# Kernel optimization log

Hardware: AMD Instinct MI355X
Metric: run time of the kernel (lower is better)

## Reference

```python
import jax, jax.numpy as jnp
import numpy as np

N_NODES = 10000
N_EDGES = 320000
NUM_NEIGHBORS = 32.0
INV_SQRT3 = 1.0 / np.sqrt(3.0)  # component-normalized CG for 1o x 1o -> 0e


def setup_inputs() -> dict:
    key = jax.random.key(0)
    ks = jax.random.split(key, 16)
    f32 = jnp.float32
    return {
        "node_input": jax.random.normal(ks[0], (N_NODES, 160), f32),   # 64x0e | 32x1o
        "node_attr": jnp.ones((N_NODES, 1), f32),                       # 1x0e
        "edge_attr": jax.random.normal(ks[1], (N_EDGES, 4), f32),       # 1x0e | 1x1o (sph harm)
        "edge_scalar_attr": jax.random.normal(ks[2], (N_EDGES, 8), f32),# radial basis
        "Wsc0": jax.random.normal(ks[3], (64, 64), f32),
        "Wsc1": jax.random.normal(ks[4], (32, 32), f32),
        "Wl1_0": jax.random.normal(ks[5], (64, 64), f32),
        "Wl1_1": jax.random.normal(ks[6], (32, 32), f32),
        "Wfc1": jax.random.normal(ks[7], (8, 64), f32),
        "Wfc2": jax.random.normal(ks[8], (64, 64), f32),
        "Wfc3": jax.random.normal(ks[9], (64, 192), f32),  # -> tp.weight_numel
        "Wl2_s": jax.random.normal(ks[10], (96, 64), f32),
        "Wl2_v": jax.random.normal(ks[11], (96, 32), f32),
        "Wa": jax.random.normal(ks[12], (96, 1), f32),
        "edge_src": jax.random.randint(ks[13], (N_EDGES,), 0, N_NODES),
        "edge_dst": jax.random.randint(ks[14], (N_EDGES,), 0, N_NODES),
    }


def _fctp_scalar_attr(xs, xv, Ws, Wv, a):
    """FullyConnectedTensorProduct(irreps, '0e', irreps) with scalar node attr a.
    xs: [N, mul_s] scalars, xv: [N, mul_v, 3] vectors. Path-normalized by 1/sqrt(fan_in)."""
    out_s = (xs @ Ws) * (a / np.sqrt(xs.shape[1]))[:, None]
    out_v = jnp.einsum('nuc,uw->nwc', xv, Wv) * (a / np.sqrt(xv.shape[1]))[:, None, None]
    return out_s, out_v


def reference(node_input, node_attr, edge_attr, edge_scalar_attr,
              Wsc0, Wsc1, Wl1_0, Wl1_1, Wfc1, Wfc2, Wfc3, Wl2_s, Wl2_v, Wa,
              edge_src, edge_dst):
    N = node_input.shape[0]
    a = node_attr[:, 0]                              # [N] scalar attr
    xs = node_input[:, :64]                          # [N,64]  64x0e
    xv = node_input[:, 64:].reshape(N, 32, 3)        # [N,32,3] 32x1o

    # self connection: FCTp(input, attr, output)
    sc_s, sc_v = _fctp_scalar_attr(xs, xv, Wsc0, Wsc1, a)
    # lin1: FCTp(input, attr, input)
    f_s, f_v = _fctp_scalar_attr(xs, xv, Wl1_0, Wl1_1, a)

    # radial MLP -> tensor-product weights [E, 192]
    h = jax.nn.gelu(edge_scalar_attr @ Wfc1 / np.sqrt(8.0))
    h = jax.nn.gelu(h @ Wfc2 / np.sqrt(64.0))
    w = h @ Wfc3 / np.sqrt(64.0)
    w0, w1, w2, w3 = w[:, :64], w[:, 64:128], w[:, 128:160], w[:, 160:192]

    # gather source node features per edge
    gs = f_s[edge_src]                               # [E,64]
    gv = f_v[edge_src]                               # [E,32,3]
    y0 = edge_attr[:, 0]                             # [E]   0e
    y1 = edge_attr[:, 1:4]                           # [E,3] 1o

    # 'uvu' tensor product, irreps_mid (sorted) = 64x0e + 32x0e + 64x1o + 32x1o
    mid0 = w0 * gs * y0[:, None]                                        # 0e x 0e -> 0e
    mid1 = w3 * jnp.einsum('euc,ec->eu', gv, y1) * INV_SQRT3            # 1o x 1o -> 0e
    mid2 = (w1 * gs)[:, :, None] * y1[:, None, :]                       # 0e x 1o -> 1o
    mid3 = w2[:, :, None] * gv * y0[:, None, None]                      # 1o x 0e -> 1o

    # scatter-add to destination nodes, normalized by sqrt(num_neighbors)
    inv = 1.0 / np.sqrt(NUM_NEIGHBORS)
    seg = lambda x: jax.ops.segment_sum(x, edge_dst, num_segments=N) * inv
    ns0, ns1, nv2, nv3 = seg(mid0), seg(mid1), seg(mid2), seg(mid3)

    mid_s = jnp.concatenate([ns0, ns1], axis=1)      # [N,96] scalars of irreps_mid
    mid_v = jnp.concatenate([nv2, nv3], axis=1)      # [N,96,3] vectors of irreps_mid

    # lin2: FCTp(mid, attr, output), fan_in = 96 for both scalar and vector outputs
    out_s = (mid_s @ Wl2_s) * (a / np.sqrt(96.0))[:, None]
    out_v = jnp.einsum('nuc,uw->nwc', mid_v, Wl2_v) * (a / np.sqrt(96.0))[:, None, None]

    # alpha: FCTp(mid, attr, '0e'); self_con output_mask is all ones here
    alpha = (mid_s @ Wa) * (a / np.sqrt(96.0))[:, None]  # [N,1]

    res_s = sc_s + alpha * out_s
    res_v = sc_v + alpha[:, :, None] * out_v
    return jnp.concatenate([res_s, res_v.reshape(N, 96)], axis=1)  # [N,160]
```

## Files before the change

kernel.cpp:

```cpp
#include <hip/hip_runtime.h>

#define N_NODES 10000
#define N_EDGES 320000
#define INV3 0.5773502691896258f

typedef short short8 __attribute__((ext_vector_type(8)));
typedef float f32x4 __attribute__((ext_vector_type(4)));

__device__ __forceinline__ float gelu_f(float x) {
    float x3 = x * x * x;
    float e = __expf(-1.5957691216057308f * (x + 0.044715f * x3));
    return x * __builtin_amdgcn_rcpf(1.0f + e);
}

__device__ __forceinline__ unsigned short f2bf(float f) {
    unsigned u = __float_as_uint(f);
    unsigned r = (u + 0x7FFFu + ((u >> 16) & 1u)) >> 16;
    return (unsigned short)r;
}
__device__ __forceinline__ float bf2f(unsigned short u) {
    return __uint_as_float(((unsigned)u) << 16);
}
__device__ __forceinline__ unsigned pk2(unsigned short lo, unsigned short hi) {
    return (unsigned)lo | ((unsigned)hi << 16);
}

__device__ __forceinline__ float rowsum16(float v) {
    v += __int_as_float(__builtin_amdgcn_update_dpp(0, __float_as_int(v), 0x118, 0xf, 0xf, true));
    v += __int_as_float(__builtin_amdgcn_update_dpp(0, __float_as_int(v), 0x114, 0xf, 0xf, true));
    v += __int_as_float(__builtin_amdgcn_update_dpp(0, __float_as_int(v), 0x112, 0xf, 0xf, true));
    v += __int_as_float(__builtin_amdgcn_update_dpp(0, __float_as_int(v), 0x111, 0xf, 0xf, true));
    return v;
}

__global__ __launch_bounds__(256) void pre_kernel(
    const int* __restrict__ edge_dst, int* __restrict__ deg,
    const float* __restrict__ Wfc1, const float* __restrict__ Wfc2,
    const float* __restrict__ Wfc3, uint4* __restrict__ fragbuf,
    const float* __restrict__ node_input, const float* __restrict__ node_attr,
    const float* __restrict__ Wl1_0, const float* __restrict__ Wl1_1,
    unsigned short* __restrict__ f_sb, unsigned short* __restrict__ f_vb)
{
    const int b = blockIdx.x;
    if (b < 1250) {
        int e = b * 256 + threadIdx.x;
        if (e < N_EDGES) atomicAdd(&deg[edge_dst[e]], 1);
        return;
    }
    if (b < 1259) {
        const int tile = (b - 1250) * 4 + (threadIdx.x >> 6);
        if (tile >= 36) return;
        const int l = threadIdx.x & 63;
        const int e = l & 15, g = l >> 4;
        unsigned p[4] = {0u, 0u, 0u, 0u};
        if (tile < 4) {
            if (g == 0) {
                #pragma unroll
                for (int j = 0; j < 8; ++j) {
                    unsigned short bb = f2bf(Wfc1[j * 64 + tile * 16 + e]);
                    p[j >> 1] |= (unsigned)bb << (16 * (j & 1));
                }
            }
        } else if (tile < 12) {
            int t2 = tile - 4; int mt = t2 >> 1, kt = t2 & 1;
            #pragma unroll
            for (int j = 0; j < 8; ++j) {
                unsigned short bb = f2bf(Wfc2[(kt * 32 + g * 8 + j) * 64 + mt * 16 + e]);
                p[j >> 1] |= (unsigned)bb << (16 * (j & 1));
            }
        } else {
            int t3 = tile - 12; int mt3 = t3 >> 1, kt = t3 & 1;
            #pragma unroll
            for (int j = 0; j < 8; ++j) {
                unsigned short bb = f2bf(Wfc3[(kt * 32 + g * 8 + j) * 192 + mt3 * 16 + e]);
                p[j >> 1] |= (unsigned)bb << (16 * (j & 1));
            }
        }
        uint4 v; v.x = p[0]; v.y = p[1]; v.z = p[2]; v.w = p[3];
        fragbuf[tile * 64 + l] = v;
        return;
    }
    const int wid = threadIdx.x >> 6;
    const int t = threadIdx.x & 63;
    const int n = (b - 1259) * 4 + wid;
    __shared__ float x[4][160];
    const float* row = node_input + (size_t)n * 160;
    for (int i = t; i < 160; i += 64) x[wid][i] = row[i];
    const float a = node_attr[n];

    float acc = 0.f;
    for (int k = 0; k < 64; ++k) acc += x[wid][k] * Wl1_0[k * 64 + t];
    f_sb[(size_t)n * 64 + t] = f2bf(acc * (a * 0.125f));

    const float sv = a * 0.17677669529663687f;
    for (int o = t; o < 96; o += 64) {
        int w = o / 3, c = o - w * 3;
        float av = 0.f;
        for (int u = 0; u < 32; ++u) av += x[wid][64 + u * 3 + c] * Wl1_1[u * 32 + w];
        f_vb[(size_t)n * 96 + o] = f2bf(av * sv);
    }
}

__global__ __launch_bounds__(256) void alloc_kernel(const int* __restrict__ deg,
                                                    int* __restrict__ gctr,
                                                    int* __restrict__ rowptr,
                                                    int* __restrict__ cursor,
                                                    int* __restrict__ bcnt) {
    const int tid = threadIdx.x;
    const int n = blockIdx.x * 256 + tid;
    const int d = (n < N_NODES) ? deg[n] : 0;

    __shared__ int part[256];
    __shared__ int blockbase;
    __shared__ int lb[64];
    part[tid] = d;
    if (tid < 64) lb[tid] = 0;
    __syncthreads();
    for (int o = 1; o < 256; o <<= 1) {
        int v = (tid >= o) ? part[tid - o] : 0;
        __syncthreads();
        part[tid] += v;
        __syncthreads();
    }
    if (tid == 255) blockbase = atomicAdd(gctr, part[255]);
    __syncthreads();
    const int base = blockbase + part[tid] - d;
    if (n < N_NODES) {
        rowptr[n] = base;
        cursor[n] = base;
        int nt = (d + 15) >> 4; if (nt > 63) nt = 63;
        atomicAdd(&lb[nt], 1);
    }
    __syncthreads();
    if (tid < 64 && lb[tid]) atomicAdd(&bcnt[tid], lb[tid]);
}

__global__ __launch_bounds__(64) void bscan_kernel(const int* __restrict__ bcnt,
                                                   int* __restrict__ bcur) {
    if (threadIdx.x == 0) {
        int run = 0;
        for (int i = 63; i >= 0; --i) { bcur[i] = run; run += bcnt[i]; }
    }
}

__global__ __launch_bounds__(256) void post_kernel(const int* __restrict__ dst,
                                                   const int* __restrict__ deg,
                                                   int* __restrict__ cursor,
                                                   int* __restrict__ elist,
                                                   int* __restrict__ bcur,
                                                   int* __restrict__ nodeperm) {
    const int b = blockIdx.x;
    if (b < 40) {
        const int tid = threadIdx.x;
        const int n = b * 256 + tid;
        __shared__ int lcnt[64], lbase[64];
        if (tid < 64) lcnt[tid] = 0;
        __syncthreads();
        int nt = 63, my = 0;
        if (n < N_NODES) {
            int d = deg[n];
            nt = (d + 15) >> 4; if (nt > 63) nt = 63;
            my = atomicAdd(&lcnt[nt], 1);
        }
        __syncthreads();
        if (tid < 64 && lcnt[tid]) lbase[tid] = atomicAdd(&bcur[tid], lcnt[tid]);
        __syncthreads();
        if (n < N_NODES) nodeperm[lbase[nt] + my] = n;
        return;
    }
    int e = (b - 40) * 256 + threadIdx.x;
    if (e < N_EDGES) {
        int p = atomicAdd(&cursor[dst[e]], 1);
        elist[p] = e;
    }
}

#define L3CHUNK(mt3_, d_) { \
    short8 a0_ = ((short8*)wfrag)[(12 + (mt3_) * 2 + 0) * 64 + l]; \
    short8 a1_ = ((short8*)wfrag)[(12 + (mt3_) * 2 + 1) * 64 + l]; \
    d_[0] = 0.f; d_[1] = 0.f; d_[2] = 0.f; d_[3] = 0.f; \
    d_ = __builtin_amdgcn_mfma_f32_16x16x32_bf16(a0_, bh0, d_, 0, 0, 0); \
    d_ = __builtin_amdgcn_mfma_f32_16x16x32_bf16(a1_, bh1, d_, 0, 0, 0); }

__global__ __launch_bounds__(256) __attribute__((amdgpu_waves_per_eu(2, 4)))
void fused_kernel(
    const float* __restrict__ edge_attr,
    const float* __restrict__ esa,
    const unsigned short* __restrict__ f_sb,
    const unsigned short* __restrict__ f_vb,
    const int* __restrict__ edge_src,
    const int* __restrict__ elist,
    const int* __restrict__ rowptr,
    const int* __restrict__ deg,
    const int* __restrict__ nodeperm,
    const float4* __restrict__ fragbuf,
    const float* __restrict__ node_input,
    const float* __restrict__ node_attr,
    const float* __restrict__ Wsc0,
    const float* __restrict__ Wsc1,
    const float* __restrict__ Wl2_s,
    const float* __restrict__ Wl2_v,
    const float* __restrict__ Wa,
    float* __restrict__ out)
{
    __shared__ __align__(16) char wfrag[36864];
    __shared__ __align__(16) char albuf[2 * 4096];
    __shared__ __align__(16) float xld[2][160];

    const int tid = threadIdx.x;
    const int l = tid & 63;
    const int wid = tid >> 6;
    const int q = wid & 1;
    const int ns = wid >> 1;

    {
        float4* w = (float4*)wfrag;
        #pragma unroll
        for (int i = 0; i < 9; ++i) w[tid + 256 * i] = fragbuf[tid + 256 * i];
    }

    const int n0 = nodeperm[blockIdx.x * 2 + 0];
    const int n1 = nodeperm[blockIdx.x * 2 + 1];
    const int n = ns ? n1 : n0;
    const int dn0 = deg[n0], dn1 = deg[n1];
    const int ntmax = ((dn0 > dn1 ? dn0 : dn1) + 15) >> 4;
    const int p0 = rowptr[n];
    const int p1 = p0 + (ns ? dn1 : dn0);
    const int p0c = p0 < N_EDGES ? p0 : N_EDGES - 1;

    if (q == 0)
        for (int i = l; i < 160; i += 64) xld[ns][i] = node_input[(size_t)n * 160 + i];

    __syncthreads();

    const int er = l & 15, gr = l >> 4;
    const int swz = (er & 7) << 4;
    char* h1b = albuf + ns * 4096;
    char* h2b = h1b + 2048;

    float acc0[2][4];
    float acc1[4];
    float acc2[2][4][3];
    float acc3[4][3];
    #pragma unroll
    for (int jj = 0; jj < 2; ++jj)
        #pragma unroll
        for (int r = 0; r < 4; ++r) {
            acc0[jj][r] = 0.f;
            acc2[jj][r][0] = 0.f; acc2[jj][r][1] = 0.f; acc2[jj][r][2] = 0.f;
        }
    #pragma unroll
    for (int r = 0; r < 4; ++r) {
        acc1[r] = 0.f;
        acc3[r][0] = 0.f; acc3[r][1] = 0.f; acc3[r][2] = 0.f;
    }

    float4 ea = {0.f, 0.f, 0.f, 0.f};
    int src = 0;
    uint4 bxu = {0u, 0u, 0u, 0u};
    if (ntmax > 0) {
        const int ci = p0 + er;
        const bool cv = ci < p1;
        const int ec = elist[cv ? ci : p0c];
        ea = ((const float4*)edge_attr)[ec];
        src = edge_src[ec];
        if (l < 16 && cv) {
            float4 xa = ((const float4*)esa)[(size_t)ec * 2 + 0];
            float4 xb = ((const float4*)esa)[(size_t)ec * 2 + 1];
            bxu.x = pk2(f2bf(xa.x), f2bf(xa.y));
            bxu.y = pk2(f2bf(xa.z), f2bf(xa.w));
            bxu.z = pk2(f2bf(xb.x), f2bf(xb.y));
            bxu.w = pk2(f2bf(xb.z), f2bf(xb.w));
        }
    }

    #pragma unroll 1
    for (int it = 0; it < ntmax; ++it) {
        const float y0 = ea.x, y1a = ea.y, y1b = ea.z, y1c = ea.w;
        union { uint4 u; short8 s; } bxc; bxc.u = bxu;
        const short8 bx = bxc.s;
        const int csrc = src;

        ushort4 gsu0 = *(const ushort4*)(f_sb + (size_t)csrc * 64 + (q * 2 + 0) * 16 + gr * 4);
        ushort4 gsu1 = *(const ushort4*)(f_sb + (size_t)csrc * 64 + (q * 2 + 1) * 16 + gr * 4);
        const unsigned short* gvp = f_vb + (size_t)csrc * 96 + (size_t)(q * 16 + gr * 4) * 3;
        ushort4 ga = *(const ushort4*)(gvp + 0);
        ushort4 gb = *(const ushort4*)(gvp + 4);
        ushort4 gc = *(const ushort4*)(gvp + 8);

        {
            const int np = p0 + (it + 1) * 16;
            const bool nv = (np + er) < p1;
            const int nec = elist[nv ? np + er : p0c];
            float4 nea = ((const float4*)edge_attr)[nec];
            int nsrc = edge_src[nec];
            uint4 nbxu = {0u, 0u, 0u, 0u};
            if (l < 16 && nv) {
                float4 xa = ((const float4*)esa)[(size_t)nec * 2 + 0];
                float4 xb = ((const float4*)esa)[(size_t)nec * 2 + 1];
                nbxu.x = pk2(f2bf(xa.x), f2bf(xa.y));
                nbxu.y = pk2(f2bf(xa.z), f2bf(xa.w));
                nbxu.z = pk2(f2bf(xb.x), f2bf(xb.y));
                nbxu.w = pk2(f2bf(xb.z), f2bf(xb.w));
            }
            ea = nea; src = nsrc; bxu = nbxu;
        }

        #pragma unroll
        for (int j = 0; j < 2; ++j) {
            const int mt = q * 2 + j;
            short8 aw = ((short8*)wfrag)[mt * 64 + l];
            f32x4 c = {0.f, 0.f, 0.f, 0.f};
            c = __builtin_amdgcn_mfma_f32_16x16x32_bf16(aw, bx, c, 0, 0, 0);
            unsigned pa = pk2(f2bf(gelu_f(c[0] * 0.35355339059327373f)),
                              f2bf(gelu_f(c[1] * 0.35355339059327373f)));
            unsigned pb = pk2(f2bf(gelu_f(c[2] * 0.35355339059327373f)),
                              f2bf(gelu_f(c[3] * 0.35355339059327373f)));
            uint2 pv; pv.x = pa; pv.y = pb;
            *(uint2*)(h1b + ((er * 128 + mt * 32 + gr * 8) ^ swz)) = pv;
        }
        __syncthreads();
        {
            short8 b0 = *(short8*)(h1b + ((er * 128 + 0  + gr * 16) ^ swz));
            short8 b1 = *(short8*)(h1b + ((er * 128 + 64 + gr * 16) ^ swz));
            #pragma unroll
            for (int j = 0; j < 2; ++j) {
                const int mt = q * 2 + j;
                short8 w2a = ((short8*)(wfrag + 4096))[(2 * mt + 0) * 64 + l];
                short8 w2b = ((short8*)(wfrag + 4096))[(2 * mt + 1) * 64 + l];
                f32x4 c = {0.f, 0.f, 0.f, 0.f};
                c = __builtin_amdgcn_mfma_f32_16x16x32_bf16(w2a, b0, c, 0, 0, 0);
                c = __builtin_amdgcn_mfma_f32_16x16x32_bf16(w2b, b1, c, 0, 0, 0);
                unsigned pa = pk2(f2bf(gelu_f(c[0] * 0.125f)), f2bf(gelu_f(c[1] * 0.125f)));
                unsigned pb = pk2(f2bf(gelu_f(c[2] * 0.125f)), f2bf(gelu_f(c[3] * 0.125f)));
                uint2 pv; pv.x = pa; pv.y = pb;
                *(uint2*)(h2b + ((er * 128 + mt * 32 + gr * 8) ^ swz)) = pv;
            }
        }
        __syncthreads();
        short8 bh0 = *(short8*)(h2b + ((er * 128 + 0  + gr * 16) ^ swz));
        short8 bh1 = *(short8*)(h2b + ((er * 128 + 64 + gr * 16) ^ swz));

        #pragma unroll
        for (int jj = 0; jj < 2; ++jj) {
            const int jg = q * 2 + jj;
            ushort4 gsu = jj ? gsu1 : gsu0;
            f32x4 gs4 = {bf2f(gsu.x), bf2f(gsu.y), bf2f(gsu.z), bf2f(gsu.w)};
            f32x4 dA; L3CHUNK(jg, dA);
            f32x4 dB; L3CHUNK(jg + 4, dB);
            #pragma unroll
            for (int r = 0; r < 4; ++r) {
                acc0[jj][r] += 0.125f * dA[r] * gs4[r] * y0;
                float t_ = 0.125f * dB[r] * gs4[r];
                acc2[jj][r][0] += t_ * y1a;
                acc2[jj][r][1] += t_ * y1b;
                acc2[jj][r][2] += t_ * y1c;
            }
        }
        {
            const int jv = q;
            float gv[12] = {bf2f(ga.x), bf2f(ga.y), bf2f(ga.z), bf2f(ga.w),
                            bf2f(gb.x), bf2f(gb.y), bf2f(gb.z), bf2f(gb.w),
                            bf2f(gc.x), bf2f(gc.y), bf2f(gc.z), bf2f(gc.w)};
            f32x4 dC; L3CHUNK(8 + jv, dC);
            f32x4 dD; L3CHUNK(10 + jv, dD);
            #pragma unroll
            for (int r = 0; r < 4; ++r) {
                float w2v = 0.125f * dC[r] * y0;
                acc3[r][0] += w2v * gv[r * 3 + 0];
                acc3[r][1] += w2v * gv[r * 3 + 1];
                acc3[r][2] += w2v * gv[r * 3 + 2];
                float dot = gv[r * 3 + 0] * y1a + gv[r * 3 + 1] * y1b + gv[r * 3 + 2] * y1c;
                acc1[r] += 0.125f * dD[r] * dot * INV3;
            }
        }
    }

    #pragma unroll
    for (int jj = 0; jj < 2; ++jj)
        #pragma unroll
        for (int r = 0; r < 4; ++r) {
            acc0[jj][r] = rowsum16(acc0[jj][r]);
            acc2[jj][r][0] = rowsum16(acc2[jj][r][0]);
            acc2[jj][r][1] = rowsum16(acc2[jj][r][1]);
            acc2[jj][r][2] = rowsum16(acc2[jj][r][2]);
        }
    #pragma unroll
    for (int r = 0; r < 4; ++r) {
        acc1[r] = rowsum16(acc1[r]);
        acc3[r][0] = rowsum16(acc3[r][0]);
        acc3[r][1] = rowsum16(acc3[r][1]);
        acc3[r][2] = rowsum16(acc3[r][2]);
    }

    __syncthreads();

    float* m = (float*)(albuf + ns * 4096);
    const float iN = 0.17677669529663687f;
    if (er == 15) {
        #pragma unroll
        for (int jj = 0; jj < 2; ++jj) {
            const int jg = q * 2 + jj;
            f32x4 v;
            v[0] = acc0[jj][0] * iN; v[1] = acc0[jj][1] * iN;
            v[2] = acc0[jj][2] * iN; v[3] = acc0[jj][3] * iN;
            *(f32x4*)(m + jg * 16 + gr * 4) = v;
        }
        {
            const int jv = q;
            f32x4 v;
            v[0] = acc1[0] * iN; v[1] = acc1[1] * iN;
            v[2] = acc1[2] * iN; v[3] = acc1[3] * iN;
            *(f32x4*)(m + 64 + jv * 16 + gr * 4) = v;
        }
        #pragma unroll
        for (int jj = 0; jj < 2; ++jj) {
            const int jg = q * 2 + jj;
            float t[12];
            #pragma unroll
            for (int r = 0; r < 4; ++r) {
                t[r * 3 + 0] = acc2[jj][r][0] * iN;
                t[r * 3 + 1] = acc2[jj][r][1] * iN;
                t[r * 3 + 2] = acc2[jj][r][2] * iN;
            }
            float* b = m + 96 + (jg * 16 + gr * 4) * 3;
            *(f32x4*)(b + 0) = (f32x4){t[0], t[1], t[2], t[3]};
            *(f32x4*)(b + 4) = (f32x4){t[4], t[5], t[6], t[7]};
            *(f32x4*)(b + 8) = (f32x4){t[8], t[9], t[10], t[11]};
        }
        {
            const int jv = q;
            float t[12];
            #pragma unroll
            for (int r = 0; r < 4; ++r) {
                t[r * 3 + 0] = acc3[r][0] * iN;
                t[r * 3 + 1] = acc3[r][1] * iN;
                t[r * 3 + 2] = acc3[r][2] * iN;
            }
            float* b = m + 288 + (jv * 16 + gr * 4) * 3;
            *(f32x4*)(b + 0) = (f32x4){t[0], t[1], t[2], t[3]};
            *(f32x4*)(b + 4) = (f32x4){t[4], t[5], t[6], t[7]};
            *(f32x4*)(b + 8) = (f32x4){t[8], t[9], t[10], t[11]};
        }
    }

    __syncthreads();

    const float a = node_attr[n];
    const float* x = xld[ns];
    const float s96 = a * 0.10206207261596575f;

    float alpha = 0.f;
    for (int i = 0; i < 96; ++i) alpha += m[i] * Wa[i];
    alpha *= s96;

    if (q == 0) {
        float outs = 0.f;
        for (int i = 0; i < 96; ++i) outs += m[i] * Wl2_s[i * 64 + l];
        outs *= s96;
        float scs = 0.f;
        for (int k = 0; k < 64; ++k) scs += x[k] * Wsc0[k * 64 + l];
        scs *= a * 0.125f;
        out[(size_t)n * 160 + l] = scs + alpha * outs;
    } else {
        const float sv = a * 0.17677669529663687f;
        for (int o = l; o < 96; o += 64) {
            int w = o / 3, c = o - w * 3;
            float ov = 0.f;
            for (int u = 0; u < 64; ++u) ov += m[96 + u * 3 + c] * Wl2_v[u * 32 + w];
            for (int u = 0; u < 32; ++u) ov += m[288 + u * 3 + c] * Wl2_v[(64 + u) * 32 + w];
            ov *= s96;
            float scv = 0.f;
            for (int u = 0; u < 32; ++u) scv += x[64 + u * 3 + c] * Wsc1[u * 32 + w];
            scv *= sv;
            out[(size_t)n * 160 + 64 + o] = scv + alpha * ov;
        }
    }
}

extern "C" void kernel_launch(void* const* d_in, const int* in_sizes, int n_in,
                              void* d_out, int out_size, void* d_ws, size_t ws_size,
                              hipStream_t stream) {
    const float* node_input = (const float*)d_in[0];
    const float* node_attr  = (const float*)d_in[1];
    const float* edge_attr  = (const float*)d_in[2];
    const float* esa        = (const float*)d_in[3];
    const float* Wsc0       = (const float*)d_in[4];
    const float* Wsc1       = (const float*)d_in[5];
    const float* Wl1_0      = (const float*)d_in[6];
    const float* Wl1_1      = (const float*)d_in[7];
    const float* Wfc1       = (const float*)d_in[8];
    const float* Wfc2       = (const float*)d_in[9];
    const float* Wfc3       = (const float*)d_in[10];
    const float* Wl2_s      = (const float*)d_in[11];
    const float* Wl2_v      = (const float*)d_in[12];
    const float* Wa         = (const float*)d_in[13];
    const int* edge_src     = (const int*)d_in[14];
    const int* edge_dst     = (const int*)d_in[15];
    float* out = (float*)d_out;

    float* ws  = (float*)d_ws;
    unsigned short* f_sb = (unsigned short*)ws;
    unsigned short* f_vb = (unsigned short*)(ws + 320000);
    uint4* fragbuf = (uint4*)(ws + 1600000);
    int* ibuf     = (int*)(ws + 1609216);
    int* deg      = ibuf;
    int* gctr     = ibuf + 10000;
    int* rowptr   = ibuf + 10016;
    int* cursor   = ibuf + 20032;
    int* elist    = ibuf + 30080;
    int* bcnt     = ibuf + 350080;
    int* bcur     = ibuf + 350144;
    int* nodeperm = ibuf + 350208;

    hipMemsetAsync(deg, 0, (size_t)(N_NODES + 1) * sizeof(int), stream);
    hipMemsetAsync(bcnt, 0, 64 * sizeof(int), stream);

    pre_kernel<<<3759, 256, 0, stream>>>(edge_dst, deg, Wfc1, Wfc2, Wfc3, fragbuf,
                                         node_input, node_attr, Wl1_0, Wl1_1, f_sb, f_vb);
    alloc_kernel<<<(N_NODES + 255) / 256, 256, 0, stream>>>(deg, gctr, rowptr, cursor, bcnt);
    bscan_kernel<<<1, 64, 0, stream>>>(bcnt, bcur);
    post_kernel<<<40 + (N_EDGES + 255) / 256, 256, 0, stream>>>(edge_dst, deg, cursor,
                                                                elist, bcur, nodeperm);

    fused_kernel<<<N_NODES / 2, 256, 0, stream>>>(edge_attr, esa, f_sb, f_vb,
                                                  edge_src, elist, rowptr, deg, nodeperm,
                                                  (const float4*)fragbuf,
                                                  node_input, node_attr,
                                                  Wsc0, Wsc1, Wl2_s, Wl2_v, Wa,
                                                  out);
}
```

Baseline: 175.8 us.

## Hold layer-3 weight fragments in registers, fold scan into alloc, use packed bf16 cvt

Each wave now loads its layer-3 MFMA weight fragments into registers once at kernel start rather than reading them from LDS on every edge. This shrinks the LDS weight buffer from 36 KB to 12 KB, and the waves-per-EU hint changes to (2,3). The bf16 packing helper is replaced with the hardware v_cvt_pk_bf16_f32 instruction. The separate bscan launch and the second memset are removed: the last alloc block, detected with a done counter, performs the bucket scan, and pre_kernel zeroes bcnt. The extra live registers may hurt occupancy, and the last-block scan depends on atomic ordering.

```diff
diff --git a/kernel.cpp b/kernel.cpp
--- a/kernel.cpp
+++ b/kernel.cpp
@@ -21,8 +21,10 @@
 __device__ __forceinline__ float bf2f(unsigned short u) {
     return __uint_as_float(((unsigned)u) << 16);
 }
-__device__ __forceinline__ unsigned pk2(unsigned short lo, unsigned short hi) {
-    return (unsigned)lo | ((unsigned)hi << 16);
+__device__ __forceinline__ unsigned cvtpk(float lo, float hi) {
+    unsigned r;
+    asm("v_cvt_pk_bf16_f32 %0, %1, %2" : "=v"(r) : "v"(lo), "v"(hi));
+    return r;
 }
 
 __device__ __forceinline__ float rowsum16(float v) {
@@ -39,7 +41,8 @@
     const float* __restrict__ Wfc3, uint4* __restrict__ fragbuf,
     const float* __restrict__ node_input, const float* __restrict__ node_attr,
     const float* __restrict__ Wl1_0, const float* __restrict__ Wl1_1,
-    unsigned short* __restrict__ f_sb, unsigned short* __restrict__ f_vb)
+    unsigned short* __restrict__ f_sb, unsigned short* __restrict__ f_vb,
+    int* __restrict__ bcnt)
 {
     const int b = blockIdx.x;
     if (b < 1250) {
@@ -48,6 +51,7 @@
         return;
     }
     if (b < 1259) {
+        if (b == 1250 && threadIdx.x < 64) bcnt[threadIdx.x] = 0;
         const int tile = (b - 1250) * 4 + (threadIdx.x >> 6);
         if (tile >= 36) return;
         const int l = threadIdx.x & 63;
@@ -103,9 +107,11 @@
 
 __global__ __launch_bounds__(256) void alloc_kernel(const int* __restrict__ deg,
                                                     int* __restrict__ gctr,
+                                                    int* __restrict__ done,
                                                     int* __restrict__ rowptr,
                                                     int* __restrict__ cursor,
-                                                    int* __restrict__ bcnt) {
+                                                    int* __restrict__ bcnt,
+                                                    int* __restrict__ bcur) {
     const int tid = threadIdx.x;
     const int n = blockIdx.x * 256 + tid;
     const int d = (n < N_NODES) ? deg[n] : 0;
@@ -113,6 +119,7 @@
     __shared__ int part[256];
     __shared__ int blockbase;
     __shared__ int lb[64];
+    __shared__ int islast;
     part[tid] = d;
     if (tid < 64) lb[tid] = 0;
     __syncthreads();
@@ -132,14 +139,16 @@
         atomicAdd(&lb[nt], 1);
     }
     __syncthreads();
-    if (tid < 64 && lb[tid]) atomicAdd(&bcnt[tid], lb[tid]);
-}
-
-__global__ __launch_bounds__(64) void bscan_kernel(const int* __restrict__ bcnt,
-                                                   int* __restrict__ bcur) {
-    if (threadIdx.x == 0) {
+    if (tid < 64 && lb[tid]) {
+        int ack = atomicAdd(&bcnt[tid], lb[tid]);
+        asm volatile("" :: "v"(ack));
+    }
+    __syncthreads();
+    if (tid == 0) islast = (atomicAdd(done, 1) == (int)gridDim.x - 1);
+    __syncthreads();
+    if (islast && tid == 0) {
         int run = 0;
-        for (int i = 63; i >= 0; --i) { bcur[i] = run; run += bcnt[i]; }
+        for (int i = 63; i >= 0; --i) { bcur[i] = run; run += atomicAdd(&bcnt[i], 0); }
     }
 }
 
@@ -175,14 +184,25 @@
     }
 }
 
-#define L3CHUNK(mt3_, d_) { \
-    short8 a0_ = ((short8*)wfrag)[(12 + (mt3_) * 2 + 0) * 64 + l]; \
-    short8 a1_ = ((short8*)wfrag)[(12 + (mt3_) * 2 + 1) * 64 + l]; \
+#define L3CHUNKR(a0_, a1_, d_) { \
     d_[0] = 0.f; d_[1] = 0.f; d_[2] = 0.f; d_[3] = 0.f; \
     d_ = __builtin_amdgcn_mfma_f32_16x16x32_bf16(a0_, bh0, d_, 0, 0, 0); \
     d_ = __builtin_amdgcn_mfma_f32_16x16x32_bf16(a1_, bh1, d_, 0, 0, 0); }
 
-__global__ __launch_bounds__(256) __attribute__((amdgpu_waves_per_eu(2, 4)))
+#define TPA(jjidx, fA0, fA1, fB0, fB1, gsu_) { \
+    f32x4 gs4 = {bf2f(gsu_.x), bf2f(gsu_.y), bf2f(gsu_.z), bf2f(gsu_.w)}; \
+    f32x4 dA; L3CHUNKR(fA0, fA1, dA); \
+    f32x4 dB; L3CHUNKR(fB0, fB1, dB); \
+    _Pragma("unroll") \
+    for (int r = 0; r < 4; ++r) { \
+        acc0[jjidx][r] += 0.125f * dA[r] * gs4[r] * y0; \
+        float t_ = 0.125f * dB[r] * gs4[r]; \
+        acc2[jjidx][r][0] += t_ * y1a; \
+        acc2[jjidx][r][1] += t_ * y1b; \
+        acc2[jjidx][r][2] += t_ * y1c; \
+    } }
+
+__global__ __launch_bounds__(256) __attribute__((amdgpu_waves_per_eu(2, 3)))
 void fused_kernel(
     const float* __restrict__ edge_attr,
     const float* __restrict__ esa,
@@ -203,7 +223,7 @@
     const float* __restrict__ Wa,
     float* __restrict__ out)
 {
-    __shared__ __align__(16) char wfrag[36864];
+    __shared__ __align__(16) char wfrag[12288];
     __shared__ __align__(16) char albuf[2 * 4096];
     __shared__ __align__(16) float xld[2][160];
 
@@ -216,8 +236,23 @@
     {
         float4* w = (float4*)wfrag;
         #pragma unroll
-        for (int i = 0; i < 9; ++i) w[tid + 256 * i] = fragbuf[tid + 256 * i];
-    }
+        for (int i = 0; i < 3; ++i) w[tid + 256 * i] = fragbuf[tid + 256 * i];
+    }
+
+    const short8* fb3 = (const short8*)fragbuf;
+    const int c0 = 2 * q, c2 = 2 * q + 4, c4 = 8 + q, c5 = 10 + q;
+    short8 w3f0  = fb3[(12 + c0 * 2 + 0) * 64 + l];
+    short8 w3f1  = fb3[(12 + c0 * 2 + 1) * 64 + l];
+    short8 w3f2  = fb3[(12 + (c0 + 1) * 2 + 0) * 64 + l];
+    short8 w3f3  = fb3[(12 + (c0 + 1) * 2 + 1) * 64 + l];
+    short8 w3f4  = fb3[(12 + c2 * 2 + 0) * 64 + l];
+    short8 w3f5  = fb3[(12 + c2 * 2 + 1) * 64 + l];
+    short8 w3f6  = fb3[(12 + (c2 + 1) * 2 + 0) * 64 + l];
+    short8 w3f7  = fb3[(12 + (c2 + 1) * 2 + 1) * 64 + l];
+    short8 w3f8  = fb3[(12 + c4 * 2 + 0) * 64 + l];
+    short8 w3f9  = fb3[(12 + c4 * 2 + 1) * 64 + l];
+    short8 w3f10 = fb3[(12 + c5 * 2 + 0) * 64 + l];
+    short8 w3f11 = fb3[(12 + c5 * 2 + 1) * 64 + l];
 
     const int n0 = nodeperm[blockIdx.x * 2 + 0];
     const int n1 = nodeperm[blockIdx.x * 2 + 1];
@@ -267,10 +302,10 @@
         if (l < 16 && cv) {
             float4 xa = ((const float4*)esa)[(size_t)ec * 2 + 0];
             float4 xb = ((const float4*)esa)[(size_t)ec * 2 + 1];
-            bxu.x = pk2(f2bf(xa.x), f2bf(xa.y));
-            bxu.y = pk2(f2bf(xa.z), f2bf(xa.w));
-            bxu.z = pk2(f2bf(xb.x), f2bf(xb.y));
-            bxu.w = pk2(f2bf(xb.z), f2bf(xb.w));
+            bxu.x = cvtpk(xa.x, xa.y);
+            bxu.y = cvtpk(xa.z, xa.w);
+            bxu.z = cvtpk(xb.x, xb.y);
+            bxu.w = cvtpk(xb.z, xb.w);
         }
     }
 
@@ -298,10 +333,10 @@
             if (l < 16 && nv) {
                 float4 xa = ((const float4*)esa)[(size_t)nec * 2 + 0];
                 float4 xb = ((const float4*)esa)[(size_t)nec * 2 + 1];
-                nbxu.x = pk2(f2bf(xa.x), f2bf(xa.y));
-                nbxu.y = pk2(f2bf(xa.z), f2bf(xa.w));
-                nbxu.z = pk2(f2bf(xb.x), f2bf(xb.y));
-                nbxu.w = pk2(f2bf(xb.z), f2bf(xb.w));
+                nbxu.x = cvtpk(xa.x, xa.y);
+                nbxu.y = cvtpk(xa.z, xa.w);
+                nbxu.z = cvtpk(xb.x, xb.y);
+                nbxu.w = cvtpk(xb.z, xb.w);
             }
             ea = nea; src = nsrc; bxu = nbxu;
         }
@@ -312,10 +347,10 @@
             short8 aw = ((short8*)wfrag)[mt * 64 + l];
             f32x4 c = {0.f, 0.f, 0.f, 0.f};
             c = __builtin_amdgcn_mfma_f32_16x16x32_bf16(aw, bx, c, 0, 0, 0);
-            unsigned pa = pk2(f2bf(gelu_f(c[0] * 0.35355339059327373f)),
-                              f2bf(gelu_f(c[1] * 0.35355339059327373f)));
-            unsigned pb = pk2(f2bf(gelu_f(c[2] * 0.35355339059327373f)),
-                              f2bf(gelu_f(c[3] * 0.35355339059327373f)));
+            unsigned pa = cvtpk(gelu_f(c[0] * 0.35355339059327373f),
+                                gelu_f(c[1] * 0.35355339059327373f));
+            unsigned pb = cvtpk(gelu_f(c[2] * 0.35355339059327373f),
+                                gelu_f(c[3] * 0.35355339059327373f));
             uint2 pv; pv.x = pa; pv.y = pb;
             *(uint2*)(h1b + ((er * 128 + mt * 32 + gr * 8) ^ swz)) = pv;
         }
@@ -331,8 +366,8 @@
                 f32x4 c = {0.f, 0.f, 0.f, 0.f};
                 c = __builtin_amdgcn_mfma_f32_16x16x32_bf16(w2a, b0, c, 0, 0, 0);
                 c = __builtin_amdgcn_mfma_f32_16x16x32_bf16(w2b, b1, c, 0, 0, 0);
-                unsigned pa = pk2(f2bf(gelu_f(c[0] * 0.125f)), f2bf(gelu_f(c[1] * 0.125f)));
-                unsigned pb = pk2(f2bf(gelu_f(c[2] * 0.125f)), f2bf(gelu_f(c[3] * 0.125f)));
+                unsigned pa = cvtpk(gelu_f(c[0] * 0.125f), gelu_f(c[1] * 0.125f));
+                unsigned pb = cvtpk(gelu_f(c[2] * 0.125f), gelu_f(c[3] * 0.125f));
                 uint2 pv; pv.x = pa; pv.y = pb;
                 *(uint2*)(h2b + ((er * 128 + mt * 32 + gr * 8) ^ swz)) = pv;
             }
@@ -341,29 +376,14 @@
         short8 bh0 = *(short8*)(h2b + ((er * 128 + 0  + gr * 16) ^ swz));
         short8 bh1 = *(short8*)(h2b + ((er * 128 + 64 + gr * 16) ^ swz));
 
-        #pragma unroll
-        for (int jj = 0; jj < 2; ++jj) {
-            const int jg = q * 2 + jj;
-            ushort4 gsu = jj ? gsu1 : gsu0;
-            f32x4 gs4 = {bf2f(gsu.x), bf2f(gsu.y), bf2f(gsu.z), bf2f(gsu.w)};
-            f32x4 dA; L3CHUNK(jg, dA);
-            f32x4 dB; L3CHUNK(jg + 4, dB);
-            #pragma unroll
-            for (int r = 0; r < 4; ++r) {
-                acc0[jj][r] += 0.125f * dA[r] * gs4[r] * y0;
-                float t_ = 0.125f * dB[r] * gs4[r];
-                acc2[jj][r][0] += t_ * y1a;
-                acc2[jj][r][1] += t_ * y1b;
-                acc2[jj][r][2] += t_ * y1c;
-            }
-        }
+        TPA(0, w3f0, w3f1, w3f4, w3f5, gsu0);
+        TPA(1, w3f2, w3f3, w3f6, w3f7, gsu1);
         {
-            const int jv = q;
             float gv[12] = {bf2f(ga.x), bf2f(ga.y), bf2f(ga.z), bf2f(ga.w),
                             bf2f(gb.x), bf2f(gb.y), bf2f(gb.z), bf2f(gb.w),
                             bf2f(gc.x), bf2f(gc.y), bf2f(gc.z), bf2f(gc.w)};
-            f32x4 dC; L3CHUNK(8 + jv, dC);
-            f32x4 dD; L3CHUNK(10 + jv, dD);
+            f32x4 dC; L3CHUNKR(w3f8, w3f9, dC);
+            f32x4 dD; L3CHUNKR(w3f10, w3f11, dD);
             #pragma unroll
             for (int r = 0; r < 4; ++r) {
                 float w2v = 0.125f * dC[r] * y0;
@@ -506,6 +526,7 @@
     int* ibuf     = (int*)(ws + 1609216);
     int* deg      = ibuf;
     int* gctr     = ibuf + 10000;
+    int* done     = ibuf + 10001;
     int* rowptr   = ibuf + 10016;
     int* cursor   = ibuf + 20032;
     int* elist    = ibuf + 30080;
@@ -513,13 +534,12 @@
     int* bcur     = ibuf + 350144;
     int* nodeperm = ibuf + 350208;
 
-    hipMemsetAsync(deg, 0, (size_t)(N_NODES + 1) * sizeof(int), stream);
-    hipMemsetAsync(bcnt, 0, 64 * sizeof(int), stream);
+    hipMemsetAsync(deg, 0, (size_t)(N_NODES + 2) * sizeof(int), stream);
 
     pre_kernel<<<3759, 256, 0, stream>>>(edge_dst, deg, Wfc1, Wfc2, Wfc3, fragbuf,
-                                         node_input, node_attr, Wl1_0, Wl1_1, f_sb, f_vb);
-    alloc_kernel<<<(N_NODES + 255) / 256, 256, 0, stream>>>(deg, gctr, rowptr, cursor, bcnt);
-    bscan_kernel<<<1, 64, 0, stream>>>(bcnt, bcur);
+                                         node_input, node_attr, Wl1_0, Wl1_1, f_sb, f_vb, bcnt);
+    alloc_kernel<<<(N_NODES + 255) / 256, 256, 0, stream>>>(deg, gctr, done, rowptr,
+                                                            cursor, bcnt, bcur);
     post_kernel<<<40 + (N_EDGES + 255) / 256, 256, 0, stream>>>(edge_dst, deg, cursor,
                                                                 elist, bcur, nodeperm);
 
```

New measurement: 205.1 us. 16.7% more time.
